# Kernel optimization log

Measured on AMD Instinct MI355X. Metric: run time of the kernel, lower is better.

## Reference

```python
import jax, jax.numpy as jnp
import numpy as np

NUM_CLASSES = 80
NUM_ANCHORS = 5
ANCHORS = np.array([1.3221, 1.73145, 3.19275, 4.00944, 5.05587, 8.09892,
                    9.47112, 4.84053, 11.2364, 10.0071], dtype=np.float32).reshape(NUM_ANCHORS, 2)
COORD_SCALE = 1.0
NOOBJECT_SCALE = 1.0
OBJECT_SCALE = 5.0
CLASS_SCALE = 1.0
SIL_THRESH = 0.6
MAX_T = 50  # max ground-truth boxes per image
NB, NH, NW = 32, 38, 38


def bbox_iou(b1, b2):
    """IoU for center-format boxes (..., 4) = (cx, cy, w, h); broadcastable.
    Matches darknet bbox_ious with x1y1x2y2=False (zero IoU if no overlap)."""
    mx = jnp.minimum(b1[..., 0] - b1[..., 2] / 2, b2[..., 0] - b2[..., 2] / 2)
    Mx = jnp.maximum(b1[..., 0] + b1[..., 2] / 2, b2[..., 0] + b2[..., 2] / 2)
    my = jnp.minimum(b1[..., 1] - b1[..., 3] / 2, b2[..., 1] - b2[..., 3] / 2)
    My = jnp.maximum(b1[..., 1] + b1[..., 3] / 2, b2[..., 1] + b2[..., 3] / 2)
    cw = b1[..., 2] + b2[..., 2] - (Mx - mx)
    ch = b1[..., 3] + b2[..., 3] - (My - my)
    inter = jnp.where((cw > 0) & (ch > 0), cw * ch, 0.0)
    union = b1[..., 2] * b1[..., 3] + b2[..., 2] * b2[..., 3] - inter
    return inter / jnp.maximum(union, 1e-12)


def setup_inputs() -> dict:
    key = jax.random.key(0)
    k1, k2, k3 = jax.random.split(key, 3)
    output = jax.random.normal(k1, (NB, NUM_ANCHORS * (5 + NUM_CLASSES), NH, NW), dtype=jnp.float32)
    # target rows: 50 boxes x (cls, x, y, w, h), normalized coords in (0,1)
    target = jax.random.uniform(k2, (NB, MAX_T * 5), dtype=jnp.float32, minval=0.02, maxval=0.98)
    features = jax.random.normal(k3, (NB, 512, NH, NW), dtype=jnp.float32)
    return {"output": output, "target": target, "features": features}


def _region_loss(output, target):
    nB, _, nH, nW = output.shape
    nA, nC = NUM_ANCHORS, NUM_CLASSES
    anchors = jnp.asarray(ANCHORS)
    sg = jax.lax.stop_gradient

    out5 = output.reshape(nB, nA, 5 + nC, nH, nW)
    x = jax.nn.sigmoid(out5[:, :, 0])
    y = jax.nn.sigmoid(out5[:, :, 1])
    w = out5[:, :, 2]
    h = out5[:, :, 3]
    conf = jax.nn.sigmoid(out5[:, :, 4])
    cls = jnp.transpose(out5[:, :, 5:], (0, 1, 3, 4, 2))  # [nB,nA,nH,nW,nC]

    # predicted boxes in grid units (detached, as pred_boxes uses .data in torch)
    grid_x = jnp.arange(nW, dtype=output.dtype)
    grid_y = jnp.arange(nH, dtype=output.dtype)
    px = sg(x) + grid_x[None, None, None, :]
    py = sg(y) + grid_y[None, None, :, None]
    pw = jnp.exp(sg(w)) * anchors[None, :, 0, None, None]
    ph = jnp.exp(sg(h)) * anchors[None, :, 1, None, None]
    pred_boxes = jnp.stack([px, py, pw, ph], axis=-1)  # [nB,nA,nH,nW,4]

    tgt = sg(target).reshape(nB, MAX_T, 5)
    gx = tgt[..., 1] * nW
    gy = tgt[..., 2] * nH
    gw = tgt[..., 3] * nW
    gh = tgt[..., 4] * nH
    # original loop breaks at first target x == 0 -> valid prefix mask
    valid = jnp.cumprod((tgt[..., 1] != 0).astype(jnp.int32), axis=1).astype(bool)

    # ---- conf_mask silencing: max IoU of every predicted box vs any GT ----
    gt_boxes = jnp.stack([gx, gy, gw, gh], axis=-1)  # [nB,50,4]
    pb_flat = pred_boxes.reshape(nB, 1, nA * nH * nW, 4)
    ious = bbox_iou(gt_boxes[:, :, None, :], pb_flat)  # [nB,50,nA*nH*nW]
    max_iou = jnp.where(valid[:, :, None], ious, 0.0).max(axis=1).reshape(nB, nA, nH, nW)
    conf_mask = jnp.where(max_iou > SIL_THRESH, 0.0, NOOBJECT_SCALE).astype(output.dtype)

    # ---- seen < 12800 warm-up branch (self.seen = 0, anchor_step = 2) ----
    shp = (nB, nA, nH, nW)
    tx = jnp.full(shp, 0.5, output.dtype)
    ty = jnp.full(shp, 0.5, output.dtype)
    tw = jnp.zeros(shp, output.dtype)
    th = jnp.zeros(shp, output.dtype)
    coord_mask = jnp.ones(shp, output.dtype)
    cls_mask = jnp.zeros(shp, output.dtype)
    tconf = jnp.zeros(shp, output.dtype)
    tcls = jnp.zeros(shp, jnp.int32)

    # ---- best anchor per GT (IoU of wh-only boxes; argmax keeps first max,
    #      matching the strict '>' update in the loop) ----
    zeros = jnp.zeros_like(gw)
    gt_wh = jnp.stack([zeros, zeros, gw, gh], axis=-1)[:, :, None, :]  # [nB,50,1,4]
    anc_wh = jnp.concatenate([jnp.zeros_like(anchors), anchors], axis=-1)[None, None]  # [1,1,nA,4]
    best_n = jnp.argmax(bbox_iou(gt_wh, anc_wh), axis=-1)  # [nB,50]

    gi = jnp.clip(jnp.floor(gx).astype(jnp.int32), 0, nW - 1)
    gj = jnp.clip(jnp.floor(gy).astype(jnp.int32), 0, nH - 1)

    b_idx = jnp.arange(nB)[:, None]
    pbox = pred_boxes[b_idx, best_n, gj, gi]  # [nB,50,4]
    iou_gt = bbox_iou(gt_boxes, pbox)  # [nB,50]

    tx_val = gx - gi.astype(output.dtype)
    ty_val = gy - gj.astype(output.dtype)
    tw_val = jnp.log(jnp.maximum(gw, 1e-12) / anchors[best_n, 0])
    th_val = jnp.log(jnp.maximum(gh, 1e-12) / anchors[best_n, 1])
    cls_val = tgt[..., 0].astype(jnp.int32)

    bi = jnp.arange(nB)

    def step(carry, t):
        coord_m, conf_m, cls_m, tx, ty, tw, th, tconf, tcls = carry
        bn = best_n[:, t]
        j = gj[:, t]
        i = gi[:, t]
        v = valid[:, t]

        def upd(arr, val):
            # indices are distinct within one step (one GT per batch element)
            old = arr[bi, bn, j, i]
            return arr.at[bi, bn, j, i].set(jnp.where(v, val, old))

        coord_m = upd(coord_m, 1.0)
        cls_m = upd(cls_m, 1.0)
        conf_m = upd(conf_m, OBJECT_SCALE)
        tx = upd(tx, tx_val[:, t])
        ty = upd(ty, ty_val[:, t])
        tw = upd(tw, tw_val[:, t])
        th = upd(th, th_val[:, t])
        tconf = upd(tconf, iou_gt[:, t])
        tcls = upd(tcls, cls_val[:, t])
        return (coord_m, conf_m, cls_m, tx, ty, tw, th, tconf, tcls), None

    init = (coord_mask, conf_mask, cls_mask, tx, ty, tw, th, tconf, tcls)
    (coord_mask, conf_mask, cls_mask, tx, ty, tw, th, tconf, tcls), _ = jax.lax.scan(
        step, init, jnp.arange(MAX_T))

    conf_mask = jnp.sqrt(conf_mask)

    loss_x = COORD_SCALE * jnp.sum((x * coord_mask - tx * coord_mask) ** 2) / 2.0
    loss_y = COORD_SCALE * jnp.sum((y * coord_mask - ty * coord_mask) ** 2) / 2.0
    loss_w = COORD_SCALE * jnp.sum((w * coord_mask - tw * coord_mask) ** 2) / 2.0
    loss_h = COORD_SCALE * jnp.sum((h * coord_mask - th * coord_mask) ** 2) / 2.0
    loss_conf = jnp.sum((conf * conf_mask - tconf * conf_mask) ** 2) / 2.0

    # sum-reduced cross entropy over cells where cls_mask == 1
    logp = jax.nn.log_softmax(cls, axis=-1)
    picked = jnp.take_along_axis(logp, tcls[..., None], axis=-1)[..., 0]
    loss_cls = -CLASS_SCALE * jnp.sum(cls_mask * picked)

    return loss_x + loss_y + loss_w + loss_h + loss_conf + loss_cls


def reference(output, target, features):
    # `features` feeds the truncated adversarial-defense tail of the original
    # forward; the detection region loss below is the complete surviving math.
    return _region_loss(output, target)
```

## Files before the change

### kernel.cpp

```cpp
#include <hip/hip_runtime.h>
#include <math.h>

#define NB 32
#define NA 5
#define NC 80
#define NH 38
#define NW 38
#define MAXT 50
#define CELLS (NH * NW)
#define CH (5 + NC)
#define NSLICE 29
#define THREADS 256
#define NWAVES (THREADS / 64)

__device__ float4 g_box[NB][MAXT];
__device__ float  g_thr[NB][MAXT];
__device__ int4   g_tgt[NB][MAXT];
__device__ float  g_corr[NB];

__device__ __constant__ float c_anchors[10] = {
    1.3221f, 1.73145f, 3.19275f, 4.00944f, 5.05587f,
    8.09892f, 9.47112f, 4.84053f, 11.2364f, 10.0071f};

__device__ __forceinline__ float sigmoidf_(float v) {
    return 1.0f / (1.0f + expf(-v));
}

__device__ __forceinline__ float bbox_iou_(float ax, float ay, float aw, float ah,
                                           float bx, float by, float bw, float bh) {
    float mx = fminf(ax - aw * 0.5f, bx - bw * 0.5f);
    float Mx = fmaxf(ax + aw * 0.5f, bx + bw * 0.5f);
    float my = fminf(ay - ah * 0.5f, by - bh * 0.5f);
    float My = fmaxf(ay + ah * 0.5f, by + bh * 0.5f);
    float cw = aw + bw - (Mx - mx);
    float ch = ah + bh - (My - my);
    float inter = (cw > 0.0f && ch > 0.0f) ? cw * ch : 0.0f;
    float uni = aw * ah + bw * bh - inter;
    return inter / fmaxf(uni, 1e-12f);
}

__device__ __forceinline__ bool hit50_(float px, float py, float pw, float ph,
                                       const float4* __restrict__ sb,
                                       const float* __restrict__ st) {
    float x1 = px - pw * 0.5f, x2 = px + pw * 0.5f;
    float y1 = py - ph * 0.5f, y2 = py + ph * 0.5f;
    float pthr = 0.375f * (pw * ph);
    bool hit = false;
    #pragma unroll
    for (int u = 0; u < MAXT; ++u) {
        float4 rb = sb[u];
        float ow = fminf(x2, rb.z) - fmaxf(x1, rb.x);
        float oh = fminf(y2, rb.w) - fmaxf(y1, rb.y);
        ow = fmaxf(ow, 0.0f);
        oh = fmaxf(oh, 0.0f);
        hit = hit | (ow * oh > pthr + st[u]);
    }
    return hit;
}

__global__ __launch_bounds__(64) void region_prep(const float* __restrict__ out,
                                                  const float* __restrict__ tgt,
                                                  float* __restrict__ loss) {
    const int b = blockIdx.x;
    const int t = threadIdx.x;
    __shared__ float4 s_box[MAXT];
    __shared__ float  s_thr[MAXT];

    const bool isrec = (t < MAXT);
    float t0 = 0.f, t1 = 0.f, gx = 0.f, gy = 0.f, gw = 0.f, gh = 0.f;
    if (isrec) {
        const float* tp = tgt + (long)b * (MAXT * 5) + t * 5;
        t0 = tp[0];
        t1 = tp[1];
        gx = t1 * NW;
        gy = tp[2] * NH;
        gw = tp[3] * NW;
        gh = tp[4] * NH;
    }
    unsigned long long nz = __ballot(isrec && (t1 != 0.0f));
    bool valid = isrec && (((~nz) & ((2ULL << t) - 1ULL)) == 0ULL);

    int bn = 0;
    float best = -1.0f;
    for (int a = 0; a < NA; ++a) {
        float aw = c_anchors[2 * a], ah = c_anchors[2 * a + 1];
        float inter = fminf(gw, aw) * fminf(gh, ah);
        float uni = gw * gh + aw * ah - inter;
        float iou = inter / fmaxf(uni, 1e-12f);
        if (iou > best) { best = iou; bn = a; }
    }
    int gi = (int)floorf(gx); gi = gi < 0 ? 0 : (gi > NW - 1 ? NW - 1 : gi);
    int gj = (int)floorf(gy); gj = gj < 0 ? 0 : (gj > NH - 1 ? NH - 1 : gj);
    int key = valid ? (bn * CELLS + gj * NW + gi) : -1;

    unsigned long long eq = 0ULL;
    for (int u = 0; u < MAXT; ++u) {
        int ku = __shfl(key, u);
        eq |= (unsigned long long)(ku == key) << u;
    }
    bool winner = valid && ((eq & ~((2ULL << t) - 1ULL)) == 0ULL);

    float4 box;
    float thr;
    if (valid) {
        box.x = gx - gw * 0.5f; box.y = gy - gh * 0.5f;
        box.z = gx + gw * 0.5f; box.w = gy + gh * 0.5f;
        thr = 0.375f * (gw * gh);
    } else {
        box.x = box.y = box.z = box.w = 0.0f;
        thr = 3e38f;
    }
    if (isrec) {
        s_box[t] = box;
        s_thr[t] = thr;
        g_box[b][t] = box;
        g_thr[b][t] = thr;
        int cls = (int)t0; cls = cls < 0 ? 0 : (cls > NC - 1 ? NC - 1 : cls);
        int4 ti;
        ti.x = winner ? 1 : 0;
        ti.y = (bn * CH + 5) * CELLS + gj * NW + gi;
        ti.z = cls;
        ti.w = 0;
        g_tgt[b][t] = ti;
    }
    __syncthreads();

    float corr = 0.0f;
    if (winner) {
        float aw = c_anchors[2 * bn], ah = c_anchors[2 * bn + 1];
        long rb = (((long)(b * NA + bn)) * CH) * CELLS + gj * NW + gi;
        float xr = out[rb];
        float yr = out[rb + CELLS];
        float wr = out[rb + 2 * CELLS];
        float hr = out[rb + 3 * CELLS];
        float cr = out[rb + 4 * CELLS];
        float sx = sigmoidf_(xr), sy = sigmoidf_(yr), sc = sigmoidf_(cr);
        float px = sx + (float)gi, py = sy + (float)gj;
        float pw = expf(wr) * aw, ph = expf(hr) * ah;
        float iou_gt = bbox_iou_(gx, gy, gw, gh, px, py, pw, ph);
        bool rhit = hit50_(px, py, pw, ph, s_box, s_thr);
        float h01 = rhit ? 0.0f : 1.0f;

        float txv = gx - (float)gi, tyv = gy - (float)gj;
        float twv = logf(fmaxf(gw, 1e-12f) / aw);
        float thv = logf(fmaxf(gh, 1e-12f) / ah);
        float dsc = sc - iou_gt;
        corr = 0.5f * ((sx - txv) * (sx - txv) - (sx - 0.5f) * (sx - 0.5f)
                     + (sy - tyv) * (sy - tyv) - (sy - 0.5f) * (sy - 0.5f)
                     + (wr - twv) * (wr - twv) - wr * wr
                     + (hr - thv) * (hr - thv) - hr * hr)
             + 0.5f * (5.0f * dsc * dsc - h01 * sc * sc);
    }
    for (int off = 32; off > 0; off >>= 1) corr += __shfl_down(corr, off);
    if (t == 0) {
        g_corr[b] = corr;
        if (b == 0) loss[0] = 0.0f;
    }
}

__global__ __launch_bounds__(THREADS) void region_main(const float* __restrict__ out,
                                                       float* __restrict__ loss) {
    const int bx = blockIdx.x;
    const int b = blockIdx.y;
    const int tid = threadIdx.x;
    const int wid = tid >> 6;
    const int lane = tid & 63;
    __shared__ float4 s_box[MAXT];
    __shared__ float  s_thr[MAXT];
    __shared__ float  s_wpart[NWAVES];

    const int idx0 = bx * THREADS + tid;
    int idx = idx0 < NA * CELLS ? idx0 : NA * CELLS - 1;
    const int a = idx / CELLS;
    const int r = idx - a * CELLS;
    const int j = r / NW;
    const int i = r - j * NW;
    const long base = (((long)(b * NA + a)) * CH) * CELLS + r;
    const float xr = out[base];
    const float yr = out[base + CELLS];
    const float wr = out[base + 2 * CELLS];
    const float hr = out[base + 3 * CELLS];
    const float cr = out[base + 4 * CELLS];

    if (tid < MAXT) {
        s_box[tid] = g_box[b][tid];
        s_thr[tid] = g_thr[b][tid];
    }

    const int gwave = bx * NWAVES + wid;
    float v0 = -INFINITY, v1 = -INFINITY, vc = 0.0f;
    bool doClass = false;
    if (gwave < MAXT) {
        const int4 ti = g_tgt[b][gwave];
        if (ti.x) {
            doClass = true;
            const float* cp = out + (long)b * (NA * CH * CELLS) + ti.y;
            v0 = cp[(long)lane * CELLS];
            v1 = (lane < NC - 64) ? cp[(long)(64 + lane) * CELLS] : -INFINITY;
            vc = cp[(long)ti.z * CELLS];
        }
    }

    __syncthreads();

    const float sx = sigmoidf_(xr), sy = sigmoidf_(yr), sc = sigmoidf_(cr);
    const float px = sx + (float)i, py = sy + (float)j;
    const float pw = expf(wr) * c_anchors[2 * a];
    const float ph = expf(hr) * c_anchors[2 * a + 1];
    const bool hit = hit50_(px, py, pw, ph, s_box, s_thr);
    float dx = sx - 0.5f, dy = sy - 0.5f;
    float cellsum = 0.5f * (dx * dx + dy * dy + wr * wr + hr * hr)
                  + (hit ? 0.0f : 0.5f * sc * sc);
    if (idx0 >= NA * CELLS) cellsum = 0.0f;

    float closs = 0.0f;
    if (doClass) {
        float m = fmaxf(v0, v1);
        for (int off = 32; off > 0; off >>= 1)
            m = fmaxf(m, __shfl_down(m, off));
        m = __shfl(m, 0);
        float e = expf(v0 - m) + ((lane < NC - 64) ? expf(v1 - m) : 0.0f);
        for (int off = 32; off > 0; off >>= 1)
            e += __shfl_down(e, off);
        if (lane == 0) closs = m + logf(e) - vc;
    }
    if (bx == 0 && tid == 0) closs += g_corr[b];

    float v = cellsum;
    for (int off = 32; off > 0; off >>= 1) v += __shfl_down(v, off);
    if (lane == 0) s_wpart[wid] = v + closs;
    __syncthreads();
    if (tid == 0) {
        float s = 0.0f;
        for (int w = 0; w < NWAVES; ++w) s += s_wpart[w];
        atomicAdd(loss, s);
    }
}

extern "C" void kernel_launch(void* const* d_in, const int* in_sizes, int n_in,
                              void* d_out, int out_size, void* d_ws, size_t ws_size,
                              hipStream_t stream) {
    const float* output = (const float*)d_in[0];
    const float* target = (const float*)d_in[1];
    float* loss = (float*)d_out;

    region_prep<<<NB, 64, 0, stream>>>(output, target, loss);
    dim3 grid(NSLICE, NB);
    region_main<<<grid, THREADS, 0, stream>>>(output, loss);
}
```

Baseline: 179.5 us.

## Split cell and class work into separate blocks, two cells per thread, deterministic finish

The main kernel now gives each thread two adjacent cells, loaded as float2, and dedicates separate blocks to the per-target class softmax. Previously class work sat inside the cell blocks and every block did an atomicAdd. Per-block partials are written to a global array and summed by a new single-block finish kernel, replacing the atomics. This cuts block count and gives wider loads, but adds a third kernel launch and serializes the final reduction.

```diff
diff --git a/kernel.cpp b/kernel.cpp
--- a/kernel.cpp
+++ b/kernel.cpp
@@ -9,14 +9,18 @@
 #define MAXT 50
 #define CELLS (NH * NW)
 #define CH (5 + NC)
-#define NSLICE 29
 #define THREADS 256
 #define NWAVES (THREADS / 64)
+#define NCELLBLK 15
+#define NCLSBLK 13
+#define NXBLK (NCELLBLK + NCLSBLK)
+#define NPAIRS 3610
 
 __device__ float4 g_box[NB][MAXT];
 __device__ float  g_thr[NB][MAXT];
 __device__ int4   g_tgt[NB][MAXT];
 __device__ float  g_corr[NB];
+__device__ float  g_part[NB][NXBLK];
 
 __device__ __constant__ float c_anchors[10] = {
     1.3221f, 1.73145f, 3.19275f, 4.00944f, 5.05587f,
@@ -58,9 +62,22 @@
     return hit;
 }
 
+__device__ __forceinline__ float cell_loss_(float xr, float yr, float wr, float hr,
+                                            float cr, int i, int j, int a,
+                                            const float4* __restrict__ sb,
+                                            const float* __restrict__ st) {
+    float sx = sigmoidf_(xr), sy = sigmoidf_(yr), sc = sigmoidf_(cr);
+    float px = sx + (float)i, py = sy + (float)j;
+    float pw = expf(wr) * c_anchors[2 * a];
+    float ph = expf(hr) * c_anchors[2 * a + 1];
+    bool hit = hit50_(px, py, pw, ph, sb, st);
+    float dx = sx - 0.5f, dy = sy - 0.5f;
+    return 0.5f * (dx * dx + dy * dy + wr * wr + hr * hr)
+         + (hit ? 0.0f : 0.5f * sc * sc);
+}
+
 __global__ __launch_bounds__(64) void region_prep(const float* __restrict__ out,
-                                                  const float* __restrict__ tgt,
-                                                  float* __restrict__ loss) {
+                                                  const float* __restrict__ tgt) {
     const int b = blockIdx.x;
     const int t = threadIdx.x;
     __shared__ float4 s_box[MAXT];
@@ -152,14 +169,10 @@
              + 0.5f * (5.0f * dsc * dsc - h01 * sc * sc);
     }
     for (int off = 32; off > 0; off >>= 1) corr += __shfl_down(corr, off);
-    if (t == 0) {
-        g_corr[b] = corr;
-        if (b == 0) loss[0] = 0.0f;
-    }
-}
-
-__global__ __launch_bounds__(THREADS) void region_main(const float* __restrict__ out,
-                                                       float* __restrict__ loss) {
+    if (t == 0) g_corr[b] = corr;
+}
+
+__global__ __launch_bounds__(THREADS) void region_main(const float* __restrict__ out) {
     const int bx = blockIdx.x;
     const int b = blockIdx.y;
     const int tid = threadIdx.x;
@@ -169,71 +182,87 @@
     __shared__ float  s_thr[MAXT];
     __shared__ float  s_wpart[NWAVES];
 
-    const int idx0 = bx * THREADS + tid;
-    int idx = idx0 < NA * CELLS ? idx0 : NA * CELLS - 1;
-    const int a = idx / CELLS;
-    const int r = idx - a * CELLS;
-    const int j = r / NW;
-    const int i = r - j * NW;
-    const long base = (((long)(b * NA + a)) * CH) * CELLS + r;
-    const float xr = out[base];
-    const float yr = out[base + CELLS];
-    const float wr = out[base + 2 * CELLS];
-    const float hr = out[base + 3 * CELLS];
-    const float cr = out[base + 4 * CELLS];
-
-    if (tid < MAXT) {
-        s_box[tid] = g_box[b][tid];
-        s_thr[tid] = g_thr[b][tid];
-    }
-
-    const int gwave = bx * NWAVES + wid;
-    float v0 = -INFINITY, v1 = -INFINITY, vc = 0.0f;
-    bool doClass = false;
-    if (gwave < MAXT) {
-        const int4 ti = g_tgt[b][gwave];
-        if (ti.x) {
-            doClass = true;
-            const float* cp = out + (long)b * (NA * CH * CELLS) + ti.y;
-            v0 = cp[(long)lane * CELLS];
-            v1 = (lane < NC - 64) ? cp[(long)(64 + lane) * CELLS] : -INFINITY;
-            vc = cp[(long)ti.z * CELLS];
-        }
-    }
-
-    __syncthreads();
-
-    const float sx = sigmoidf_(xr), sy = sigmoidf_(yr), sc = sigmoidf_(cr);
-    const float px = sx + (float)i, py = sy + (float)j;
-    const float pw = expf(wr) * c_anchors[2 * a];
-    const float ph = expf(hr) * c_anchors[2 * a + 1];
-    const bool hit = hit50_(px, py, pw, ph, s_box, s_thr);
-    float dx = sx - 0.5f, dy = sy - 0.5f;
-    float cellsum = 0.5f * (dx * dx + dy * dy + wr * wr + hr * hr)
-                  + (hit ? 0.0f : 0.5f * sc * sc);
-    if (idx0 >= NA * CELLS) cellsum = 0.0f;
-
-    float closs = 0.0f;
-    if (doClass) {
-        float m = fmaxf(v0, v1);
-        for (int off = 32; off > 0; off >>= 1)
-            m = fmaxf(m, __shfl_down(m, off));
-        m = __shfl(m, 0);
-        float e = expf(v0 - m) + ((lane < NC - 64) ? expf(v1 - m) : 0.0f);
-        for (int off = 32; off > 0; off >>= 1)
-            e += __shfl_down(e, off);
-        if (lane == 0) closs = m + logf(e) - vc;
-    }
-    if (bx == 0 && tid == 0) closs += g_corr[b];
-
-    float v = cellsum;
+    if (bx < NCELLBLK) {
+        const int p0 = bx * THREADS + tid;
+        const int p = p0 < NPAIRS ? p0 : NPAIRS - 1;
+        const int c0 = 2 * p;
+        const int a = c0 / CELLS;
+        const int r0 = c0 - a * CELLS;
+        const int j = r0 / NW;
+        const int i0 = r0 - j * NW;
+        const long base = (((long)(b * NA + a)) * CH) * CELLS + r0;
+
+        const float2 x2 = *(const float2*)&out[base];
+        const float2 y2 = *(const float2*)&out[base + CELLS];
+        const float2 w2 = *(const float2*)&out[base + 2 * CELLS];
+        const float2 h2 = *(const float2*)&out[base + 3 * CELLS];
+        const float2 q2 = *(const float2*)&out[base + 4 * CELLS];
+
+        if (tid < MAXT) {
+            s_box[tid] = g_box[b][tid];
+            s_thr[tid] = g_thr[b][tid];
+        }
+        __syncthreads();
+
+        float cs = cell_loss_(x2.x, y2.x, w2.x, h2.x, q2.x, i0,     j, a, s_box, s_thr)
+                 + cell_loss_(x2.y, y2.y, w2.y, h2.y, q2.y, i0 + 1, j, a, s_box, s_thr);
+        if (p0 >= NPAIRS) cs = 0.0f;
+
+        for (int off = 32; off > 0; off >>= 1) cs += __shfl_down(cs, off);
+        if (lane == 0) s_wpart[wid] = cs;
+        __syncthreads();
+        if (tid == 0) {
+            float s = 0.0f;
+            for (int w = 0; w < NWAVES; ++w) s += s_wpart[w];
+            g_part[b][bx] = s;
+        }
+    } else {
+        const int rec = __builtin_amdgcn_readfirstlane((bx - NCELLBLK) * NWAVES + wid);
+        float closs = 0.0f;
+        if (rec < MAXT) {
+            const int4 ti = g_tgt[b][rec];
+            if (ti.x) {
+                const float* cp = out + (long)b * (NA * CH * CELLS) + ti.y;
+                float v0 = cp[(long)lane * CELLS];
+                float v1 = (lane < NC - 64) ? cp[(long)(64 + lane) * CELLS] : -INFINITY;
+                float vc = cp[(long)ti.z * CELLS];
+                float m = fmaxf(v0, v1);
+                for (int off = 32; off > 0; off >>= 1)
+                    m = fmaxf(m, __shfl_down(m, off));
+                m = __shfl(m, 0);
+                float e = expf(v0 - m) + ((lane < NC - 64) ? expf(v1 - m) : 0.0f);
+                for (int off = 32; off > 0; off >>= 1)
+                    e += __shfl_down(e, off);
+                if (lane == 0) closs = m + logf(e) - vc;
+            }
+        }
+        if (lane == 0) s_wpart[wid] = closs;
+        __syncthreads();
+        if (tid == 0) {
+            float s = 0.0f;
+            for (int w = 0; w < NWAVES; ++w) s += s_wpart[w];
+            g_part[b][bx] = s;
+        }
+    }
+}
+
+__global__ __launch_bounds__(1024) void region_finish(float* __restrict__ loss) {
+    const int tid = threadIdx.x;
+    const int wid = tid >> 6;
+    const int lane = tid & 63;
+    __shared__ float sp[16];
+
+    float v = 0.0f;
+    if (tid < NB * NXBLK) v = ((const float*)g_part)[tid];
+    if (tid < NB) v += g_corr[tid];
+
     for (int off = 32; off > 0; off >>= 1) v += __shfl_down(v, off);
-    if (lane == 0) s_wpart[wid] = v + closs;
+    if (lane == 0) sp[wid] = v;
     __syncthreads();
     if (tid == 0) {
         float s = 0.0f;
-        for (int w = 0; w < NWAVES; ++w) s += s_wpart[w];
-        atomicAdd(loss, s);
+        for (int w = 0; w < 16; ++w) s += sp[w];
+        loss[0] = s;
     }
 }
 
@@ -244,7 +273,8 @@
     const float* target = (const float*)d_in[1];
     float* loss = (float*)d_out;
 
-    region_prep<<<NB, 64, 0, stream>>>(output, target, loss);
-    dim3 grid(NSLICE, NB);
-    region_main<<<grid, THREADS, 0, stream>>>(output, loss);
-}
+    region_prep<<<NB, 64, 0, stream>>>(output, target);
+    dim3 grid(NXBLK, NB);
+    region_main<<<grid, THREADS, 0, stream>>>(output);
+    region_finish<<<1, 1024, 0, stream>>>(loss);
+}
```

Result: no change. 176.0 us (-1.9%).
